# Kernel tuning notes

Hardware: AMD Instinct MI355X
Metric: run time of the kernel (lower is better)

Reference implementation:

```python
import jax, jax.numpy as jnp
import numpy as np

FEAT, HW, C, M, U, B = 2048, 14, 20, 64, 128, 4


def _grid_sample_one(img, grid):
    # img: [M, H, W]; grid: [H, W, 2] normalized coords (x, y), align_corners=True, zero padding
    H, W = img.shape[-2], img.shape[-1]
    gx = (grid[..., 0] + 1.0) * 0.5 * (W - 1)
    gy = (grid[..., 1] + 1.0) * 0.5 * (H - 1)
    x0 = jnp.floor(gx).astype(jnp.int32); x1 = x0 + 1
    y0 = jnp.floor(gy).astype(jnp.int32); y1 = y0 + 1

    def gather(yi, xi):
        valid = (yi >= 0) & (yi < H) & (xi >= 0) & (xi < W)
        yc = jnp.clip(yi, 0, H - 1); xc = jnp.clip(xi, 0, W - 1)
        return img[:, yc, xc] * valid.astype(img.dtype)  # [M, H, W]

    w00 = (x1 - gx) * (y1 - gy); w01 = (gx - x0) * (y1 - gy)
    w10 = (x1 - gx) * (gy - y0); w11 = (gx - x0) * (gy - y0)
    return (gather(y0, x0) * w00 + gather(y0, x1) * w01 +
            gather(y1, x0) * w10 + gather(y1, x1) * w11)


def setup_inputs() -> dict:
    key = jax.random.key(0)
    ks = jax.random.split(key, 5)
    x = jax.random.normal(ks[0], (B, FEAT, HW, HW), jnp.float32)
    W_parcel = jax.random.normal(ks[1], (C, M, FEAT), jnp.float32) * 0.02
    W_stn = jax.random.normal(ks[2], (C, 6, M * (HW // 2) ** 2), jnp.float32) * 1e-3
    b_stn = jnp.tile(jnp.array([1.0, 0.0, 0.0, 0.0, 1.0, 0.0], jnp.float32), (C, 1))
    Wg = jax.random.normal(ks[3], (C, C - 1, U, 2 * M), jnp.float32) * 0.02
    w_phi = jax.random.normal(ks[4], (1, U), jnp.float32) * 0.05
    b_phi = jnp.zeros((1,), jnp.float32)
    return {"x": x, "W_parcel": W_parcel, "W_stn": W_stn, "b_stn": b_stn,
            "Wg": Wg, "w_phi": w_phi, "b_phi": b_phi}


def reference(x, W_parcel, W_stn, b_stn, Wg, w_phi, b_phi):
    b, _, H, W = x.shape
    # per-class 1x1 conv parcels: [B, C, M, H, W]
    x_tmp = jnp.einsum('bfhw,cmf->bcmhw', x, W_parcel)
    # relu + 2x2 maxpool -> [B, C, M, 7, 7]
    pooled = jax.nn.relu(x_tmp).reshape(b, C, M, H // 2, 2, W // 2, 2).max(axis=(4, 6))
    flat = pooled.reshape(b, C, M * (H // 2) * (W // 2))
    theta = (jnp.einsum('bck,cjk->bcj', flat, W_stn) + b_stn).reshape(b, C, 2, 3)
    # affine grid (align_corners=True): base[h, w] = [x_norm, y_norm, 1]
    xs = jnp.linspace(-1.0, 1.0, W); ys = jnp.linspace(-1.0, 1.0, H)
    base = jnp.stack(jnp.broadcast_arrays(xs[None, :], ys[:, None], jnp.ones((H, W))), -1)
    grid = jnp.einsum('bcij,hwj->bchwi', theta, base)  # [B, C, H, W, 2]
    # STN sampling of the pre-relu parcel maps
    x_obj = jax.vmap(jax.vmap(_grid_sample_one))(x_tmp, grid)  # [B, C, M, H, W]
    # pairwise relation: relu(Wa[i,j] x_obj[i] + Wb[i,j] x_obj[j]) summed over j != i
    jidx = jnp.asarray(np.array([[k for k in range(C) if k != c] for c in range(C)]))
    Wa, Wb = Wg[..., :M], Wg[..., M:]
    A = jnp.einsum('ckum,bcmhw->bckuhw', Wa, x_obj)
    Bp = jnp.einsum('ckum,bckmhw->bckuhw', Wb, x_obj[:, jidx])
    rel = jax.nn.relu(A + Bp).sum(axis=2)          # [B, C, U, H, W]
    rel_mean = rel.mean(axis=(-2, -1))             # [B, C, U]  (adaptive avg pool 1x1)
    out = jnp.einsum('bcu,ou->bco', rel_mean, w_phi)[..., 0] + b_phi  # [B, C]
    return out
```

## Files before the change

### kernel.cpp

```cpp
#include <hip/hip_runtime.h>

#define FEAT 2048
#define HWD 14
#define NPIX 196
#define C_CLS 20
#define M_DIM 64
#define U_DIM 128
#define B_SZ 4
#define K_REL 19
#define NPOOL 49

typedef __attribute__((ext_vector_type(8))) short bf16x8s;
typedef __attribute__((ext_vector_type(8))) unsigned short ushort8v;
typedef __attribute__((ext_vector_type(4))) float f32x4;
typedef __attribute__((ext_vector_type(4))) unsigned int uint4v;

__device__ inline unsigned short f2bf(float f) {
    unsigned u = __builtin_bit_cast(unsigned, f);
    unsigned r = (u + 0x7FFF + ((u >> 16) & 1)) >> 16;
    return (unsigned short)r;
}

__device__ inline bf16x8s cvt8(const float* __restrict__ p) {
    float4 lo = *(const float4*)p;
    float4 hi = *(const float4*)(p + 4);
    bf16x8s r;
    r[0] = (short)f2bf(lo.x); r[1] = (short)f2bf(lo.y);
    r[2] = (short)f2bf(lo.z); r[3] = (short)f2bf(lo.w);
    r[4] = (short)f2bf(hi.x); r[5] = (short)f2bf(hi.y);
    r[6] = (short)f2bf(hi.z); r[7] = (short)f2bf(hi.w);
    return r;
}

__global__ __launch_bounds__(256) void prep_kernel(
        const float* __restrict__ x, const float* __restrict__ Wg,
        const float* __restrict__ Wp,
        unsigned short* __restrict__ xts, unsigned short* __restrict__ Wgb,
        unsigned short* __restrict__ Awp) {
    __shared__ unsigned short T[64][210];
    const int blk = blockIdx.x;
    const int tid = threadIdx.x;
    if (blk < 128) {
        const int b = blk >> 5;
        const int s = blk & 31;
        const float* xb = x + ((size_t)b * FEAT + s * 64) * NPIX;
        for (int i = tid; i < 64 * NPIX; i += 256) {
            int kk = i / NPIX, hw = i - kk * NPIX;
            T[kk][hw] = f2bf(xb[(size_t)kk * NPIX + hw]);
        }
        __syncthreads();
        unsigned short* ob = xts + ((size_t)(b * 32 + s)) * 1664 * 8;
        for (int i = tid; i < 1664; i += 256) {
            int ch = i / 208, row = i - ch * 208;
            ushort8v o;
#pragma unroll
            for (int j = 0; j < 8; j++)
                o[j] = (row < NPIX) ? T[ch * 8 + j][row] : (unsigned short)0;
            *(ushort8v*)(ob + (size_t)i * 8) = o;
        }
    } else {
        const int lane = tid & 63;
        int gw = (blk - 128) * 4 + (tid >> 6);
        for (int r = gw; r < 5120; r += 896 * 4) {
            int c = r >> 8;
            int rem = r & 255;
            int s = rem >> 3, fi = rem & 7;
            int rt = fi >> 1, f = fi & 1;
            int m = rt * 16 + (lane & 15);
            int k = s * 64 + f * 32 + (lane >> 4) * 8;
            bf16x8s v = cvt8(Wp + ((size_t)(c * M_DIM + m)) * FEAT + k);
            *(bf16x8s*)(Awp + ((size_t)r * 64 + lane) * 8) = v;
        }
        const int NWG4 = C_CLS * K_REL * U_DIM * 2 * M_DIM / 4;
        for (int gi = (blk - 128) * 256 + tid; gi < NWG4; gi += 896 * 256) {
            float4 v = *(const float4*)(Wg + (size_t)gi * 4);
            ushort4 o;
            o.x = f2bf(v.x); o.y = f2bf(v.y); o.z = f2bf(v.z); o.w = f2bf(v.w);
            *(ushort4*)(Wgb + (size_t)gi * 4) = o;
        }
    }
}

__global__ __launch_bounds__(512) void fused_kernel(
        const unsigned short* __restrict__ xts,
        const unsigned short* __restrict__ Awp,
        const float* __restrict__ Wstn,
        const float* __restrict__ bstn,
        unsigned short* __restrict__ x_objT) {
    __shared__ __align__(16) char smem[78336];
    float* xs     = (float*)smem;
    float* pooled = (float*)(smem + 53504);
    float* red    = (float*)(smem + 66048);

    const int c = blockIdx.x, b = blockIdx.y;
    const int tid = threadIdx.x;
    const int lane = tid & 63, wv = tid >> 6;
    const int l15 = lane & 15, lq = lane >> 4;
    const int t0 = (wv < 5) ? 2 * wv : 10 + (wv - 5);
    const int nt = (wv < 5) ? 2 : 1;

    const unsigned short* xsrc = xts + (size_t)b * 32 * 1664 * 8;
    const unsigned short* asrc = Awp + (size_t)c * 256 * 64 * 8;

    bf16x8s A0[8], A1[8], B0[4], B1[4];
    auto aload = [&](int s, bf16x8s (&A)[8]) {
#pragma unroll
        for (int fi = 0; fi < 8; fi++)
            A[fi] = *(const bf16x8s*)(asrc + (((size_t)s * 8 + fi) * 64 + lane) * 8);
    };
    auto bload = [&](int s, bf16x8s (&B)[4]) {
#pragma unroll
        for (int q = 0; q < 2; q++) {
            if (q < nt) {
#pragma unroll
                for (int f = 0; f < 2; f++)
                    B[q * 2 + f] = *(const bf16x8s*)(xsrc +
                        ((size_t)s * 1664 + (f * 4 + lq) * 208 + (t0 + q) * 16 + l15) * 8);
            }
        }
    };

    f32x4 acc[2][4];
#pragma unroll
    for (int q = 0; q < 2; q++)
#pragma unroll
        for (int rt = 0; rt < 4; rt++) acc[q][rt] = (f32x4){0.f, 0.f, 0.f, 0.f};

    auto compute = [&](bf16x8s (&A)[8], bf16x8s (&B)[4]) {
#pragma unroll
        for (int q = 0; q < 2; q++) {
            if (q < nt) {
#pragma unroll
                for (int rt = 0; rt < 4; rt++)
#pragma unroll
                    for (int f = 0; f < 2; f++)
                        acc[q][rt] = __builtin_amdgcn_mfma_f32_16x16x32_bf16(
                            A[rt * 2 + f], B[q * 2 + f], acc[q][rt], 0, 0, 0);
            }
        }
    };

    aload(0, A0); bload(0, B0);
    for (int sp = 0; sp < 16; sp++) {
        aload(2 * sp + 1, A1); bload(2 * sp + 1, B1);
        compute(A0, B0);
        if (sp < 15) { aload(2 * sp + 2, A0); bload(2 * sp + 2, B0); }
        compute(A1, B1);
    }

#pragma unroll
    for (int q = 0; q < 2; q++) {
        if (q < nt) {
            int tt = t0 + q;
#pragma unroll
            for (int rt = 0; rt < 4; rt++)
#pragma unroll
                for (int r = 0; r < 4; r++)
                    xs[(rt * 16 + lq * 4 + r) * 209 + tt * 16 + l15] = acc[q][rt][r];
        }
    }
    __syncthreads();

    for (int i = tid; i < 3136; i += 512) {
        int m = i / NPOOL, p = i - m * NPOOL;
        int ph = p / 7, pw = p - ph * 7;
        const float* bp = &xs[m * 209 + ph * 2 * HWD + pw * 2];
        float v = fmaxf(fmaxf(bp[0], bp[1]), fmaxf(bp[HWD], bp[HWD + 1]));
        pooled[i] = fmaxf(v, 0.f);
    }
    __syncthreads();

    float sj[6] = {0, 0, 0, 0, 0, 0};
#pragma unroll
    for (int it = 0; it < 7; it++) {
        int kk = tid + it * 512;
        if (kk < 3136) {
            float f = pooled[kk];
#pragma unroll
            for (int j = 0; j < 6; j++)
                sj[j] += f * Wstn[((size_t)c * 6 + j) * 3136 + kk];
        }
    }
#pragma unroll
    for (int j = 0; j < 6; j++) red[j * 512 + tid] = sj[j];
    __syncthreads();
    for (int off = 256; off > 0; off >>= 1) {
        if (tid < off) {
#pragma unroll
            for (int j = 0; j < 6; j++)
                red[j * 512 + tid] += red[j * 512 + tid + off];
        }
        __syncthreads();
    }
    float th[6];
#pragma unroll
    for (int j = 0; j < 6; j++) th[j] = red[j * 512] + bstn[c * 6 + j];

    const int m = tid & 63;
    const int hwg = tid >> 6;
    unsigned short* ob = x_objT + ((size_t)(b * C_CLS + c) * NPIX) * 64 + m;
    const float* xrow = &xs[m * 209];
    for (int it = 0; it < 25; it++) {
        int hw = hwg + it * 8;
        if (hw >= NPIX) break;
        int h = hw / HWD, w = hw - h * HWD;
        float fx = -1.f + w * (2.f / 13.f);
        float fy = -1.f + h * (2.f / 13.f);
        float gxn = th[0] * fx + th[1] * fy + th[2];
        float gyn = th[3] * fx + th[4] * fy + th[5];
        float gx = (gxn + 1.f) * 0.5f * (HWD - 1);
        float gy = (gyn + 1.f) * 0.5f * (HWD - 1);
        float x0f = floorf(gx), y0f = floorf(gy);
        int x0 = (int)x0f, y0 = (int)y0f;
        int x1 = x0 + 1, y1 = y0 + 1;
        auto gat = [&](int yi, int xi) -> float {
            bool v = (yi >= 0) & (yi < HWD) & (xi >= 0) & (xi < HWD);
            int yc = min(max(yi, 0), HWD - 1);
            int xc = min(max(xi, 0), HWD - 1);
            return v ? xrow[yc * HWD + xc] : 0.f;
        };
        float xw1 = (float)x1 - gx, xw0 = gx - (float)x0;
        float yw1 = (float)y1 - gy, yw0 = gy - (float)y0;
        float val = gat(y0, x0) * xw1 * yw1 + gat(y0, x1) * xw0 * yw1 +
                    gat(y1, x0) * xw1 * yw0 + gat(y1, x1) * xw0 * yw0;
        ob[(size_t)hw * 64] = f2bf(val);
    }
}

#define MP 136
__global__ __launch_bounds__(256) void relation_mfma_kernel(
        const unsigned short* __restrict__ x_objT,
        const unsigned short* __restrict__ Wgb,
        float* __restrict__ partial) {
    __shared__ unsigned short Xs[208 * MP];
    const int k = blockIdx.x;
    const int c = blockIdx.y;
    const int b = blockIdx.z;
    const int kj = (k < c) ? k : k + 1;
    const int tid = threadIdx.x;
    const int lane = tid & 63;
    const int wv = tid >> 6;
    const int l15 = lane & 15;
    const int lq = lane >> 4;

    bf16x8s AF[2][4];
    const unsigned short* wgb = Wgb + (((size_t)c * K_REL + k) * U_DIM) * (2 * M_DIM);
#pragma unroll
    for (int ut = 0; ut < 2; ut++) {
        int u = wv * 32 + ut * 16 + l15;
#pragma unroll
        for (int ks = 0; ks < 4; ks++)
            AF[ut][ks] = *(const bf16x8s*)(wgb + (size_t)u * 128 + ks * 32 + lq * 8);
    }

    const unsigned short* xc = x_objT + ((size_t)(b * C_CLS + c)) * NPIX * 64;
    const unsigned short* xk = x_objT + ((size_t)(b * C_CLS + kj)) * NPIX * 64;
#pragma unroll
    for (int it = 0; it < 13; it++) {
        int i = tid + it * 256;
        int hw = i >> 4, ch = i & 15;
        uint4v v = {0, 0, 0, 0};
        if (hw < NPIX) {
            const unsigned short* src = (ch < 8 ? xc : xk) + (size_t)hw * 64 + (ch & 7) * 8;
            v = *(const uint4v*)src;
        }
        *(uint4v*)(&Xs[hw * MP + ch * 8]) = v;
    }
    __syncthreads();

    float csum[2][4];
#pragma unroll
    for (int ut = 0; ut < 2; ut++)
#pragma unroll
        for (int r = 0; r < 4; r++) csum[ut][r] = 0.f;

    for (int t = 0; t < 13; t++) {
        bf16x8s BF[4];
#pragma unroll
        for (int ks = 0; ks < 4; ks++)
            BF[ks] = *(const bf16x8s*)(&Xs[(t * 16 + l15) * MP + ks * 32 + lq * 8]);
        f32x4 acc0 = {0.f, 0.f, 0.f, 0.f}, acc1 = {0.f, 0.f, 0.f, 0.f};
#pragma unroll
        for (int ks = 0; ks < 4; ks++) {
            acc0 = __builtin_amdgcn_mfma_f32_16x16x32_bf16(AF[0][ks], BF[ks], acc0, 0, 0, 0);
            acc1 = __builtin_amdgcn_mfma_f32_16x16x32_bf16(AF[1][ks], BF[ks], acc1, 0, 0, 0);
        }
#pragma unroll
        for (int r = 0; r < 4; r++) {
            csum[0][r] += fmaxf(acc0[r], 0.f);
            csum[1][r] += fmaxf(acc1[r], 0.f);
        }
    }
#pragma unroll
    for (int mask = 1; mask < 16; mask <<= 1) {
#pragma unroll
        for (int ut = 0; ut < 2; ut++)
#pragma unroll
            for (int r = 0; r < 4; r++)
                csum[ut][r] += __shfl_xor(csum[ut][r], mask, 64);
    }
    if (l15 == 0) {
        float* pp = partial + (((size_t)b * C_CLS + c) * K_REL + k) * U_DIM;
#pragma unroll
        for (int ut = 0; ut < 2; ut++)
#pragma unroll
            for (int r = 0; r < 4; r++)
                pp[wv * 32 + ut * 16 + lq * 4 + r] = csum[ut][r];
    }
}

__global__ __launch_bounds__(128) void final_kernel(
        const float* __restrict__ partial, const float* __restrict__ wphi,
        const float* __restrict__ bphi, float* __restrict__ out) {
    int bc = blockIdx.x;
    int u = threadIdx.x;
    float s = 0.f;
    for (int k = 0; k < K_REL; k++)
        s += partial[((size_t)bc * K_REL + k) * U_DIM + u];
    s *= wphi[u];
    __shared__ float red[128];
    red[u] = s;
    __syncthreads();
    for (int off = 64; off > 0; off >>= 1) {
        if (u < off) red[u] += red[u + off];
        __syncthreads();
    }
    if (u == 0) out[bc] = red[0] / (float)NPIX + bphi[0];
}

extern "C" void kernel_launch(void* const* d_in, const int* in_sizes, int n_in,
                              void* d_out, int out_size, void* d_ws, size_t ws_size,
                              hipStream_t stream) {
    const float* x    = (const float*)d_in[0];
    const float* Wp   = (const float*)d_in[1];
    const float* Wstn = (const float*)d_in[2];
    const float* bstn = (const float*)d_in[3];
    const float* Wg   = (const float*)d_in[4];
    const float* wphi = (const float*)d_in[5];
    const float* bphi = (const float*)d_in[6];
    float* out = (float*)d_out;
    char* wsb = (char*)d_ws;

    unsigned short* xts    = (unsigned short*)(wsb);
    unsigned short* Wgb    = (unsigned short*)(wsb + 3407872);
    unsigned short* Awp    = (unsigned short*)(wsb + 15859712);
    unsigned short* x_objT = (unsigned short*)(wsb + 21102592);
    float* partial         = (float*)(wsb + 23109632);

    prep_kernel<<<1024, 256, 0, stream>>>(x, Wg, Wp, xts, Wgb, Awp);
    fused_kernel<<<dim3(C_CLS, B_SZ), 512, 0, stream>>>(xts, Awp, Wstn, bstn, x_objT);
    relation_mfma_kernel<<<dim3(K_REL, C_CLS, B_SZ), 256, 0, stream>>>(x_objT, Wgb, partial);
    final_kernel<<<80, 128, 0, stream>>>(partial, wphi, bphi, out);
}
```

Before: 77.28 us.

## Split parcel GEMM over K into separate kernel and drop Wg bf16 prepass

```diff
diff --git a/kernel.cpp b/kernel.cpp
--- a/kernel.cpp
+++ b/kernel.cpp
@@ -33,10 +33,8 @@
 }
 
 __global__ __launch_bounds__(256) void prep_kernel(
-        const float* __restrict__ x, const float* __restrict__ Wg,
-        const float* __restrict__ Wp,
-        unsigned short* __restrict__ xts, unsigned short* __restrict__ Wgb,
-        unsigned short* __restrict__ Awp) {
+        const float* __restrict__ x, const float* __restrict__ Wp,
+        unsigned short* __restrict__ xts, unsigned short* __restrict__ Awp) {
     __shared__ unsigned short T[64][210];
     const int blk = blockIdx.x;
     const int tid = threadIdx.x;
@@ -61,7 +59,7 @@
     } else {
         const int lane = tid & 63;
         int gw = (blk - 128) * 4 + (tid >> 6);
-        for (int r = gw; r < 5120; r += 896 * 4) {
+        for (int r = gw; r < 5120; r += 160 * 4) {
             int c = r >> 8;
             int rem = r & 255;
             int s = rem >> 3, fi = rem & 7;
@@ -71,19 +69,87 @@
             bf16x8s v = cvt8(Wp + ((size_t)(c * M_DIM + m)) * FEAT + k);
             *(bf16x8s*)(Awp + ((size_t)r * 64 + lane) * 8) = v;
         }
-        const int NWG4 = C_CLS * K_REL * U_DIM * 2 * M_DIM / 4;
-        for (int gi = (blk - 128) * 256 + tid; gi < NWG4; gi += 896 * 256) {
-            float4 v = *(const float4*)(Wg + (size_t)gi * 4);
-            ushort4 o;
-            o.x = f2bf(v.x); o.y = f2bf(v.y); o.z = f2bf(v.z); o.w = f2bf(v.w);
-            *(ushort4*)(Wgb + (size_t)gi * 4) = o;
-        }
-    }
-}
-
-__global__ __launch_bounds__(512) void fused_kernel(
+    }
+}
+
+__global__ __launch_bounds__(256) void gemm_kernel(
         const unsigned short* __restrict__ xts,
         const unsigned short* __restrict__ Awp,
+        float* __restrict__ xsp) {
+    const int c = blockIdx.x, b = blockIdx.y, ks = blockIdx.z;
+    const int tid = threadIdx.x;
+    const int lane = tid & 63, wv = tid >> 6;
+    const int l15 = lane & 15, lq = lane >> 4;
+    const int t0 = (wv == 0) ? 0 : (3 * wv + 1);
+    const int nt = (wv == 0) ? 4 : 3;
+
+    const unsigned short* xsrc = xts + (size_t)b * 32 * 1664 * 8;
+    const unsigned short* asrc = Awp + (size_t)c * 256 * 64 * 8;
+    const int s0 = ks * 8;
+
+    bf16x8s A0[8], A1[8], B0[8], B1[8];
+    auto aload = [&](int s, bf16x8s (&A)[8]) {
+#pragma unroll
+        for (int fi = 0; fi < 8; fi++)
+            A[fi] = *(const bf16x8s*)(asrc + (((size_t)s * 8 + fi) * 64 + lane) * 8);
+    };
+    auto bload = [&](int s, bf16x8s (&B)[8]) {
+#pragma unroll
+        for (int q = 0; q < 4; q++) {
+            if (q < nt) {
+#pragma unroll
+                for (int f = 0; f < 2; f++)
+                    B[q * 2 + f] = *(const bf16x8s*)(xsrc +
+                        ((size_t)s * 1664 + (f * 4 + lq) * 208 + (t0 + q) * 16 + l15) * 8);
+            }
+        }
+    };
+
+    f32x4 acc[4][4];
+#pragma unroll
+    for (int q = 0; q < 4; q++)
+#pragma unroll
+        for (int rt = 0; rt < 4; rt++) acc[q][rt] = (f32x4){0.f, 0.f, 0.f, 0.f};
+
+    auto compute = [&](bf16x8s (&A)[8], bf16x8s (&B)[8]) {
+#pragma unroll
+        for (int q = 0; q < 4; q++) {
+            if (q < nt) {
+#pragma unroll
+                for (int rt = 0; rt < 4; rt++)
+#pragma unroll
+                    for (int f = 0; f < 2; f++)
+                        acc[q][rt] = __builtin_amdgcn_mfma_f32_16x16x32_bf16(
+                            A[rt * 2 + f], B[q * 2 + f], acc[q][rt], 0, 0, 0);
+            }
+        }
+    };
+
+    aload(s0, A0); bload(s0, B0);
+#pragma unroll
+    for (int sp = 0; sp < 4; sp++) {
+        aload(s0 + 2 * sp + 1, A1); bload(s0 + 2 * sp + 1, B1);
+        compute(A0, B0);
+        if (sp < 3) { aload(s0 + 2 * sp + 2, A0); bload(s0 + 2 * sp + 2, B0); }
+        compute(A1, B1);
+    }
+
+    float* ob = xsp + ((size_t)(ks * B_SZ + b) * C_CLS + c) * 64 * 208;
+#pragma unroll
+    for (int q = 0; q < 4; q++) {
+        if (q < nt) {
+            int tt = t0 + q;
+#pragma unroll
+            for (int rt = 0; rt < 4; rt++)
+#pragma unroll
+                for (int r = 0; r < 4; r++)
+                    ob[(rt * 16 + lq * 4 + r) * 208 + tt * 16 + l15] = acc[q][rt][r];
+        }
+    }
+}
+
+__global__ __launch_bounds__(512) void phases_kernel(
+        const float* __restrict__ xsp,
         const float* __restrict__ Wstn,
         const float* __restrict__ bstn,
         unsigned short* __restrict__ x_objT) {
@@ -94,70 +160,14 @@
 
     const int c = blockIdx.x, b = blockIdx.y;
     const int tid = threadIdx.x;
-    const int lane = tid & 63, wv = tid >> 6;
-    const int l15 = lane & 15, lq = lane >> 4;
-    const int t0 = (wv < 5) ? 2 * wv : 10 + (wv - 5);
-    const int nt = (wv < 5) ? 2 : 1;
-
-    const unsigned short* xsrc = xts + (size_t)b * 32 * 1664 * 8;
-    const unsigned short* asrc = Awp + (size_t)c * 256 * 64 * 8;
-
-    bf16x8s A0[8], A1[8], B0[4], B1[4];
-    auto aload = [&](int s, bf16x8s (&A)[8]) {
-#pragma unroll
-        for (int fi = 0; fi < 8; fi++)
-            A[fi] = *(const bf16x8s*)(asrc + (((size_t)s * 8 + fi) * 64 + lane) * 8);
-    };
-    auto bload = [&](int s, bf16x8s (&B)[4]) {
-#pragma unroll
-        for (int q = 0; q < 2; q++) {
-            if (q < nt) {
-#pragma unroll
-                for (int f = 0; f < 2; f++)
-                    B[q * 2 + f] = *(const bf16x8s*)(xsrc +
-                        ((size_t)s * 1664 + (f * 4 + lq) * 208 + (t0 + q) * 16 + l15) * 8);
-            }
-        }
-    };
-
-    f32x4 acc[2][4];
-#pragma unroll
-    for (int q = 0; q < 2; q++)
-#pragma unroll
-        for (int rt = 0; rt < 4; rt++) acc[q][rt] = (f32x4){0.f, 0.f, 0.f, 0.f};
-
-    auto compute = [&](bf16x8s (&A)[8], bf16x8s (&B)[4]) {
-#pragma unroll
-        for (int q = 0; q < 2; q++) {
-            if (q < nt) {
-#pragma unroll
-                for (int rt = 0; rt < 4; rt++)
-#pragma unroll
-                    for (int f = 0; f < 2; f++)
-                        acc[q][rt] = __builtin_amdgcn_mfma_f32_16x16x32_bf16(
-                            A[rt * 2 + f], B[q * 2 + f], acc[q][rt], 0, 0, 0);
-            }
-        }
-    };
-
-    aload(0, A0); bload(0, B0);
-    for (int sp = 0; sp < 16; sp++) {
-        aload(2 * sp + 1, A1); bload(2 * sp + 1, B1);
-        compute(A0, B0);
-        if (sp < 15) { aload(2 * sp + 2, A0); bload(2 * sp + 2, B0); }
-        compute(A1, B1);
-    }
-
-#pragma unroll
-    for (int q = 0; q < 2; q++) {
-        if (q < nt) {
-            int tt = t0 + q;
-#pragma unroll
-            for (int rt = 0; rt < 4; rt++)
-#pragma unroll
-                for (int r = 0; r < 4; r++)
-                    xs[(rt * 16 + lq * 4 + r) * 209 + tt * 16 + l15] = acc[q][rt][r];
-        }
+
+    const size_t S = (size_t)B_SZ * C_CLS * 13312;
+    const float* pb = xsp + (size_t)(b * C_CLS + c) * 13312;
+#pragma unroll 2
+    for (int it = 0; it < 26; it++) {
+        int i = tid + it * 512;
+        float v = pb[i] + pb[i + S] + pb[i + 2 * S] + pb[i + 3 * S];
+        xs[(i / 208) * 209 + (i % 208)] = v;
     }
     __syncthreads();
 
@@ -196,9 +206,13 @@
 #pragma unroll
     for (int j = 0; j < 6; j++) th[j] = red[j * 512] + bstn[c * 6 + j];
 
+    unsigned short* obase = x_objT + ((size_t)(b * C_CLS + c) * 208) * 64;
+    for (int i = tid; i < 12 * 64; i += 512)
+        obase[(size_t)(NPIX + i / 64) * 64 + (i & 63)] = 0;
+
     const int m = tid & 63;
     const int hwg = tid >> 6;
-    unsigned short* ob = x_objT + ((size_t)(b * C_CLS + c) * NPIX) * 64 + m;
+    unsigned short* ob = obase + m;
     const float* xrow = &xs[m * 209];
     for (int it = 0; it < 25; it++) {
         int hw = hwg + it * 8;
@@ -227,12 +241,10 @@
     }
 }
 
-#define MP 136
 __global__ __launch_bounds__(256) void relation_mfma_kernel(
         const unsigned short* __restrict__ x_objT,
-        const unsigned short* __restrict__ Wgb,
+        const float* __restrict__ Wg,
         float* __restrict__ partial) {
-    __shared__ unsigned short Xs[208 * MP];
     const int k = blockIdx.x;
     const int c = blockIdx.y;
     const int b = blockIdx.z;
@@ -244,29 +256,17 @@
     const int lq = lane >> 4;
 
     bf16x8s AF[2][4];
-    const unsigned short* wgb = Wgb + (((size_t)c * K_REL + k) * U_DIM) * (2 * M_DIM);
+    const float* wgb = Wg + (((size_t)c * K_REL + k) * U_DIM) * (2 * M_DIM);
 #pragma unroll
     for (int ut = 0; ut < 2; ut++) {
         int u = wv * 32 + ut * 16 + l15;
 #pragma unroll
         for (int ks = 0; ks < 4; ks++)
-            AF[ut][ks] = *(const bf16x8s*)(wgb + (size_t)u * 128 + ks * 32 + lq * 8);
-    }
-
-    const unsigned short* xc = x_objT + ((size_t)(b * C_CLS + c)) * NPIX * 64;
-    const unsigned short* xk = x_objT + ((size_t)(b * C_CLS + kj)) * NPIX * 64;
-#pragma unroll
-    for (int it = 0; it < 13; it++) {
-        int i = tid + it * 256;
-        int hw = i >> 4, ch = i & 15;
-        uint4v v = {0, 0, 0, 0};
-        if (hw < NPIX) {
-            const unsigned short* src = (ch < 8 ? xc : xk) + (size_t)hw * 64 + (ch & 7) * 8;
-            v = *(const uint4v*)src;
-        }
-        *(uint4v*)(&Xs[hw * MP + ch * 8]) = v;
-    }
-    __syncthreads();
+            AF[ut][ks] = cvt8(wgb + (size_t)u * 128 + ks * 32 + lq * 8);
+    }
+
+    const unsigned short* xc = x_objT + ((size_t)(b * C_CLS + c)) * 208 * 64;
+    const unsigned short* xk = x_objT + ((size_t)(b * C_CLS + kj)) * 208 * 64;
 
     float csum[2][4];
 #pragma unroll
@@ -277,8 +277,11 @@
     for (int t = 0; t < 13; t++) {
         bf16x8s BF[4];
 #pragma unroll
-        for (int ks = 0; ks < 4; ks++)
-            BF[ks] = *(const bf16x8s*)(&Xs[(t * 16 + l15) * MP + ks * 32 + lq * 8]);
+        for (int ks = 0; ks < 4; ks++) {
+            const unsigned short* base = (ks < 2) ? xc : xk;
+            BF[ks] = *(const bf16x8s*)(base + (size_t)(t * 16 + l15) * 64
+                                       + (ks & 1) * 32 + lq * 8);
+        }
         f32x4 acc0 = {0.f, 0.f, 0.f, 0.f}, acc1 = {0.f, 0.f, 0.f, 0.f};
 #pragma unroll
         for (int ks = 0; ks < 4; ks++) {
@@ -342,13 +345,14 @@
     char* wsb = (char*)d_ws;
 
     unsigned short* xts    = (unsigned short*)(wsb);
-    unsigned short* Wgb    = (unsigned short*)(wsb + 3407872);
-    unsigned short* Awp    = (unsigned short*)(wsb + 15859712);
-    unsigned short* x_objT = (unsigned short*)(wsb + 21102592);
-    float* partial         = (float*)(wsb + 23109632);
-
-    prep_kernel<<<1024, 256, 0, stream>>>(x, Wg, Wp, xts, Wgb, Awp);
-    fused_kernel<<<dim3(C_CLS, B_SZ), 512, 0, stream>>>(xts, Awp, Wstn, bstn, x_objT);
-    relation_mfma_kernel<<<dim3(K_REL, C_CLS, B_SZ), 256, 0, stream>>>(x_objT, Wgb, partial);
+    unsigned short* Awp    = (unsigned short*)(wsb + 3407872);
+    float* xsp             = (float*)(wsb + 8650752);
+    unsigned short* x_objT = (unsigned short*)(wsb + 25690112);
+    float* partial         = (float*)(wsb + 27820032);
+
+    prep_kernel<<<288, 256, 0, stream>>>(x, Wp, xts, Awp);
+    gemm_kernel<<<dim3(C_CLS, B_SZ, 4), 256, 0, stream>>>(xts, Awp, xsp);
+    phases_kernel<<<dim3(C_CLS, B_SZ), 512, 0, stream>>>(xsp, Wstn, bstn, x_objT);
+    relation_mfma_kernel<<<dim3(K_REL, C_CLS, B_SZ), 256, 0, stream>>>(x_objT, Wg, partial);
     final_kernel<<<80, 128, 0, stream>>>(partial, wphi, bphi, out);
 }
```

After: 100.0 us. 1.29x slower.
